# Performance work log

Hardware: AMD Instinct MI355X
Metric: run time of the kernel (lower is better)

The kernel has to match this reference:

```python
import jax, jax.numpy as jnp
import numpy as np

N, E = 50000, 800000          # nodes, edges
F_IN, H, C = 32, 64, 7        # input feats, hidden, classes
EPS = 1e-5                    # BatchNorm eps


def setup_inputs() -> dict:
    key = jax.random.key(0)
    ks = jax.random.split(key, 16)
    inp = {
        "x": jax.random.normal(ks[0], (N, F_IN), jnp.float32),
        "edge_index": jax.random.randint(ks[1], (2, E), 0, N),
        "edge_attr": jax.random.uniform(ks[2], (E, 1), jnp.float32),
    }

    def conv_params(k, cin, cout, i):
        k1, k2 = jax.random.split(k)
        s = 1.0 / np.sqrt(cin)
        inp[f"W{i}"] = jax.random.uniform(k1, (2, cin, cout), jnp.float32, -s, s)  # spline kernel weights
        inp[f"R{i}"] = jax.random.uniform(k2, (cin, cout), jnp.float32, -s, s)     # root weight
        inp[f"B{i}"] = jnp.zeros((cout,), jnp.float32)

    conv_params(ks[3], F_IN, H, 0)
    conv_params(ks[4], H, H, 1)
    conv_params(ks[5], H, C, 2)
    for i in range(2):  # BatchNorm (eval mode: running stats)
        inp[f"G{i}"] = jnp.ones((H,), jnp.float32)
        inp[f"BE{i}"] = jnp.zeros((H,), jnp.float32)
        inp[f"RM{i}"] = 0.1 * jax.random.normal(ks[6 + 2 * i], (H,), jnp.float32)
        inp[f"RV{i}"] = jax.random.uniform(ks[7 + 2 * i], (H,), jnp.float32, 0.5, 1.5)
    return inp


def spline_conv(x, src, dst, u, W, R, B):
    # dim=1, kernel_size=2, degree=1 open B-spline:
    # basis = (1-u, u) with weight indices (0, 1) for u in [0,1).
    basis = jnp.stack([1.0 - u, u], axis=1)               # [E, 2]
    msg = jnp.einsum('ec,ek,kco->eo', x[src], basis, W)    # gather + basis-weighted linear
    agg = jax.ops.segment_sum(msg, dst, num_segments=N)    # scatter-add
    deg = jax.ops.segment_sum(jnp.ones((src.shape[0],), x.dtype), dst, num_segments=N)
    agg = agg / jnp.maximum(deg, 1.0)[:, None]             # aggr='mean' (default)
    return agg + x @ R + B                                 # root weight + bias


def batch_norm(x, g, b, rm, rv):
    return (x - rm) * jax.lax.rsqrt(rv + EPS) * g + b


def reference(x, edge_index, edge_attr,
              W0, R0, B0, W1, R1, B1, W2, R2, B2,
              G0, BE0, RM0, RV0, G1, BE1, RM1, RV1):
    src, dst = edge_index[0], edge_index[1]
    u = edge_attr[:, 0]
    h = spline_conv(x, src, dst, u, W0, R0, B0)
    h = jax.nn.elu(batch_norm(h, G0, BE0, RM0, RV0))
    h = spline_conv(h, src, dst, u, W1, R1, B1)
    h = jax.nn.elu(batch_norm(h, G1, BE1, RM1, RV1))
    h = spline_conv(h, src, dst, u, W2, R2, B2)
    return jax.nn.log_softmax(h, axis=1)
```

## Files before the change

kernel.cpp:

```cpp
#include <hip/hip_runtime.h>
#include <hip/hip_fp16.h>
#include <math.h>

#define NN 50000
#define NE 800000
#define EPSV 1e-5f
#define BSHIFT 7
#define BSIZE 128
#define NB 391
#define CAP 2560

typedef _Float16 h2f   __attribute__((ext_vector_type(2)));
typedef _Float16 f16x8 __attribute__((ext_vector_type(8)));
typedef float    f32x4 __attribute__((ext_vector_type(4)));

__global__ __launch_bounds__(64) void prep_all_kernel(
        const float* __restrict__ W0, const float* __restrict__ R0,
        const float* __restrict__ W1, const float* __restrict__ R1,
        const float* __restrict__ W2, const float* __restrict__ R2,
        const float* __restrict__ B0, const float* __restrict__ B1,
        const float* __restrict__ G0, const float* __restrict__ BE0,
        const float* __restrict__ RM0, const float* __restrict__ RV0,
        const float* __restrict__ G1, const float* __restrict__ BE1,
        const float* __restrict__ RM1, const float* __restrict__ RV1,
        __half* __restrict__ Bf0, __half* __restrict__ Bf1, __half* __restrict__ Bf7,
        float* __restrict__ bn0, float* __restrict__ bn1,
        int* __restrict__ bcursor) {
    int lane = threadIdx.x;
    int bid = blockIdx.x;
    int c = lane & 15;
    int kbase = ((lane >> 4) << 3);
    _Float16 vals[8];
    if (bid < 12) {
        int ks = bid >> 2, nt = bid & 3;
        int n = nt * 16 + c;
#pragma unroll
        for (int j = 0; j < 8; ++j) {
            int kg = ks * 32 + kbase + j;
            float v = (kg < 64) ? W0[(kg & 1) * 2048 + (kg >> 1) * 64 + n]
                                : R0[(kg - 64) * 64 + n];
            vals[j] = (_Float16)v;
        }
        *reinterpret_cast<f16x8*>(Bf0 + ((size_t)(bid * 64 + lane)) * 8) =
            *reinterpret_cast<f16x8*>(vals);
    } else if (bid < 36) {
        int t = bid - 12;
        int ks = t >> 2, nt = t & 3;
        int n = nt * 16 + c;
#pragma unroll
        for (int j = 0; j < 8; ++j) {
            int kg = ks * 32 + kbase + j;
            float v = (kg < 128) ? W1[(kg & 1) * 4096 + (kg >> 1) * 64 + n]
                                 : R1[(kg - 128) * 64 + n];
            vals[j] = (_Float16)v;
        }
        *reinterpret_cast<f16x8*>(Bf1 + ((size_t)(t * 64 + lane)) * 8) =
            *reinterpret_cast<f16x8*>(vals);
    } else if (bid < 40) {
        int ksnt = bid - 36;
        int ks = ksnt >> 1, nt = ksnt & 1;
#pragma unroll
        for (int j = 0; j < 8; ++j) {
            int k = ks * 32 + kbase + j;
            float v = 0.f;
            if (nt == 0) {
                if (c < 7)                 v = W2[k * 7 + c];
                else if (c >= 8 && c < 15) v = W2[448 + k * 7 + (c - 8)];
            } else {
                if (c < 7)                 v = R2[k * 7 + c];
            }
            vals[j] = (_Float16)v;
        }
        *reinterpret_cast<f16x8*>(Bf7 + ((size_t)(ksnt * 64 + lane)) * 8) =
            *reinterpret_cast<f16x8*>(vals);
    } else if (bid == 40) {
        float s = G0[lane] * rsqrtf(RV0[lane] + EPSV);
        bn0[lane] = s;
        bn0[64 + lane] = B0[lane] * s + BE0[lane] - RM0[lane] * s;
    } else if (bid == 41) {
        float s = G1[lane] * rsqrtf(RV1[lane] + EPSV);
        bn1[lane] = s;
        bn1[64 + lane] = B1[lane] * s + BE1[lane] - RM1[lane] * s;
    } else {
        int b = (bid - 42) * 64 + lane;
        if (b < NB) bcursor[b] = b * CAP;
    }
}

__global__ __launch_bounds__(256) void binB_xh_kernel(
        const int* __restrict__ src, const int* __restrict__ dst,
        const float* __restrict__ attr, int* __restrict__ bcursor,
        unsigned* __restrict__ es1su, unsigned char* __restrict__ es1dl, int E,
        const float* __restrict__ x, __half* __restrict__ xh) {
    __shared__ int hist[NB];
    __shared__ int base[NB];
    if (blockIdx.x >= NB) {
        int t = (blockIdx.x - NB) * 256 + threadIdx.x;
        size_t idx = (size_t)t * 8;
        if (idx < (size_t)NN * 32) {
            float4 f0 = *reinterpret_cast<const float4*>(x + idx);
            float4 f1 = *reinterpret_cast<const float4*>(x + idx + 4);
            _Float16 v[8] = {(_Float16)f0.x, (_Float16)f0.y, (_Float16)f0.z, (_Float16)f0.w,
                             (_Float16)f1.x, (_Float16)f1.y, (_Float16)f1.z, (_Float16)f1.w};
            *reinterpret_cast<f16x8*>(xh + idx) = *reinterpret_cast<f16x8*>(v);
        }
        return;
    }
    for (int i = threadIdx.x; i < NB; i += blockDim.x) hist[i] = 0;
    __syncthreads();
    const int chunk = (E + NB - 1) / NB;
    int e0 = blockIdx.x * chunk;
    int e1 = e0 + chunk; if (e1 > E) e1 = E;
    unsigned su[8]; unsigned char dlv[8]; short bv[8];
#pragma unroll
    for (int j = 0; j < 8; ++j) {
        int e = e0 + threadIdx.x + j * 256;
        if (e < e1) {
            int d = dst[e];
            int b = d >> BSHIFT;
            __half uh = __float2half_rn(attr[e]);
            su[j]  = ((unsigned)src[e] << 16) | (unsigned)__half_as_ushort(uh);
            dlv[j] = (unsigned char)(d & (BSIZE - 1));
            bv[j]  = (short)b;
            atomicAdd(&hist[b], 1);
        }
    }
    __syncthreads();
    for (int i = threadIdx.x; i < NB; i += blockDim.x) {
        int cnt = hist[i];
        base[i] = cnt ? atomicAdd(&bcursor[i], cnt) : 0;
        hist[i] = 0;
    }
    __syncthreads();
#pragma unroll
    for (int j = 0; j < 8; ++j) {
        int e = e0 + threadIdx.x + j * 256;
        if (e < e1) {
            int b = bv[j];
            int slot = base[b] + atomicAdd(&hist[b], 1);
            es1su[slot] = su[j];
            es1dl[slot] = dlv[j];
        }
    }
}

__global__ __launch_bounds__(256) void placeC_kernel(const int* __restrict__ bcursor,
                                                     const unsigned* __restrict__ es1su,
                                                     const unsigned char* __restrict__ es1dl,
                                                     int2* __restrict__ rowrange,
                                                     uint2* __restrict__ es8) {
    __shared__ int hist[BSIZE];
    __shared__ int stmp[BSIZE];
    __shared__ int cur[BSIZE];
    int b = blockIdx.x;
    int t = threadIdx.x;
    int bs = b * CAP;
    int be = bcursor[b];
    if (t < BSIZE) hist[t] = 0;
    __syncthreads();
    unsigned su[10]; unsigned char dlv[10];
#pragma unroll
    for (int j = 0; j < 10; ++j) {
        int i = bs + t + j * 256;
        if (i < be) {
            su[j]  = es1su[i];
            dlv[j] = es1dl[i];
            atomicAdd(&hist[dlv[j]], 1);
        }
    }
    __syncthreads();
    if (t < BSIZE) {
        int v = hist[t];
        int incl = v;
#pragma unroll
        for (int o = 1; o < 64; o <<= 1) {
            int nv = __shfl_up(incl, o, 64);
            if ((t & 63) >= o) incl += nv;
        }
        stmp[t] = incl;
    }
    __syncthreads();
    if (t < BSIZE) {
        int excl = stmp[t] - hist[t] + ((t >= 64) ? stmp[63] : 0);
        cur[t] = excl;
        int node = b * BSIZE + t;
        if (node < NN) {
            int2 rr; rr.x = bs + excl; rr.y = bs + excl + hist[t];
            rowrange[node] = rr;
        }
    }
    __syncthreads();
#pragma unroll
    for (int j = 0; j < 10; ++j) {
        int i = bs + t + j * 256;
        if (i < be) {
            unsigned r = su[j];
            int dl = dlv[j];
            int slot = bs + atomicAdd(&cur[dl], 1);
            __half uh = __ushort_as_half((unsigned short)(r & 0xffffu));
            __half2 p = __halves2half2(__hsub(__ushort_as_half((unsigned short)0x3C00u), uh), uh);
            uint2 rec;
            rec.x = r >> 16;
            rec.y = *reinterpret_cast<unsigned*>(&p);
            es8[slot] = rec;
        }
    }
}

__global__ __launch_bounds__(256) void gatherS32_kernel(const int2* __restrict__ rowrange,
                                                        const uint2* __restrict__ es8,
                                                        const __half* __restrict__ xh,
                                                        __half* __restrict__ S, int n_nodes) {
    int n = (blockIdx.x * blockDim.x + threadIdx.x) >> 6;
    int lane = threadIdx.x & 63;
    if (n >= n_nodes) return;
    int2 rr = rowrange[n];
    int beg = __builtin_amdgcn_readfirstlane(rr.x);
    int end = __builtin_amdgcn_readfirstlane(rr.y);
    int c = lane & 31;
    const __half* xb = xh + c;
    float a0 = 0.f, a1 = 0.f, a2 = 0.f, a3 = 0.f;
    float b0 = 0.f, b1 = 0.f, b2 = 0.f, b3 = 0.f;
    int i = beg + (lane >> 5);
    for (; i + 6 < end; i += 8) {
        uint2 q0 = es8[i];
        uint2 q1 = es8[i + 2];
        uint2 q2 = es8[i + 4];
        uint2 q3 = es8[i + 6];
        float x0 = __half2float(xb[(size_t)q0.x << 5]);
        float x1 = __half2float(xb[(size_t)q1.x << 5]);
        float x2 = __half2float(xb[(size_t)q2.x << 5]);
        float x3 = __half2float(xb[(size_t)q3.x << 5]);
        __half2 u0 = __builtin_bit_cast(__half2, q0.y);
        __half2 u1 = __builtin_bit_cast(__half2, q1.y);
        __half2 u2 = __builtin_bit_cast(__half2, q2.y);
        __half2 u3 = __builtin_bit_cast(__half2, q3.y);
        a0 = fmaf(__low2float(u0), x0, a0); b0 = fmaf(__high2float(u0), x0, b0);
        a1 = fmaf(__low2float(u1), x1, a1); b1 = fmaf(__high2float(u1), x1, b1);
        a2 = fmaf(__low2float(u2), x2, a2); b2 = fmaf(__high2float(u2), x2, b2);
        a3 = fmaf(__low2float(u3), x3, a3); b3 = fmaf(__high2float(u3), x3, b3);
    }
    for (; i < end; i += 2) {
        uint2 q = es8[i];
        float xv = __half2float(xb[(size_t)q.x << 5]);
        __half2 u = __builtin_bit_cast(__half2, q.y);
        a0 = fmaf(__low2float(u), xv, a0); b0 = fmaf(__high2float(u), xv, b0);
    }
    float a = (a0 + a1) + (a2 + a3);
    float b = (b0 + b1) + (b2 + b3);
    a += __shfl_xor(a, 32);
    b += __shfl_xor(b, 32);
    float degv = (float)(end - beg);
    if (degv < 1.f) degv = 1.f;
    float inv = 1.f / degv;
    if (lane < 32) {
        reinterpret_cast<__half2*>(S + (size_t)n * 64)[c] = __floats2half2_rn(a * inv, b * inv);
    }
}

__global__ __launch_bounds__(256) void gatherS64_kernel(const int2* __restrict__ rowrange,
                                                        const uint2* __restrict__ es8,
                                                        const __half* __restrict__ ht,
                                                        __half* __restrict__ S, int n_nodes) {
    int n = (blockIdx.x * blockDim.x + threadIdx.x) >> 6;
    int lane = threadIdx.x & 63;
    if (n >= n_nodes) return;
    int2 rr = rowrange[n];
    int beg = __builtin_amdgcn_readfirstlane(rr.x);
    int end = __builtin_amdgcn_readfirstlane(rr.y);
    const __half* xb = ht + lane;
    float a0 = 0.f, a1 = 0.f, a2 = 0.f, a3 = 0.f;
    float b0 = 0.f, b1 = 0.f, b2 = 0.f, b3 = 0.f;
    int i = beg;
    if (i < end && (i & 1)) {
        uint2 q = es8[i];
        float xv = __half2float(xb[(size_t)q.x << 6]);
        __half2 u = __builtin_bit_cast(__half2, q.y);
        a0 = fmaf(__low2float(u), xv, a0); b0 = fmaf(__high2float(u), xv, b0);
        ++i;
    }
    for (; i + 7 < end; i += 8) {
        uint4 p0 = *reinterpret_cast<const uint4*>(es8 + i);
        uint4 p1 = *reinterpret_cast<const uint4*>(es8 + i + 2);
        uint4 p2 = *reinterpret_cast<const uint4*>(es8 + i + 4);
        uint4 p3 = *reinterpret_cast<const uint4*>(es8 + i + 6);
        float x0 = __half2float(xb[(size_t)p0.x << 6]);
        float x1 = __half2float(xb[(size_t)p0.z << 6]);
        float x2 = __half2float(xb[(size_t)p1.x << 6]);
        float x3 = __half2float(xb[(size_t)p1.z << 6]);
        float x4 = __half2float(xb[(size_t)p2.x << 6]);
        float x5 = __half2float(xb[(size_t)p2.z << 6]);
        float x6 = __half2float(xb[(size_t)p3.x << 6]);
        float x7 = __half2float(xb[(size_t)p3.z << 6]);
        __half2 u0 = __builtin_bit_cast(__half2, p0.y);
        __half2 u1 = __builtin_bit_cast(__half2, p0.w);
        __half2 u2 = __builtin_bit_cast(__half2, p1.y);
        __half2 u3 = __builtin_bit_cast(__half2, p1.w);
        __half2 u4 = __builtin_bit_cast(__half2, p2.y);
        __half2 u5 = __builtin_bit_cast(__half2, p2.w);
        __half2 u6 = __builtin_bit_cast(__half2, p3.y);
        __half2 u7 = __builtin_bit_cast(__half2, p3.w);
        a0 = fmaf(__low2float(u0), x0, a0); b0 = fmaf(__high2float(u0), x0, b0);
        a1 = fmaf(__low2float(u1), x1, a1); b1 = fmaf(__high2float(u1), x1, b1);
        a2 = fmaf(__low2float(u2), x2, a2); b2 = fmaf(__high2float(u2), x2, b2);
        a3 = fmaf(__low2float(u3), x3, a3); b3 = fmaf(__high2float(u3), x3, b3);
        a0 = fmaf(__low2float(u4), x4, a0); b0 = fmaf(__high2float(u4), x4, b0);
        a1 = fmaf(__low2float(u5), x5, a1); b1 = fmaf(__high2float(u5), x5, b1);
        a2 = fmaf(__low2float(u6), x6, a2); b2 = fmaf(__high2float(u6), x6, b2);
        a3 = fmaf(__low2float(u7), x7, a3); b3 = fmaf(__high2float(u7), x7, b3);
    }
    for (; i + 1 < end; i += 2) {
        uint4 p = *reinterpret_cast<const uint4*>(es8 + i);
        float x0 = __half2float(xb[(size_t)p.x << 6]);
        float x1 = __half2float(xb[(size_t)p.z << 6]);
        __half2 u0 = __builtin_bit_cast(__half2, p.y);
        __half2 u1 = __builtin_bit_cast(__half2, p.w);
        a0 = fmaf(__low2float(u0), x0, a0); b0 = fmaf(__high2float(u0), x0, b0);
        a1 = fmaf(__low2float(u1), x1, a1); b1 = fmaf(__high2float(u1), x1, b1);
    }
    if (i < end) {
        uint2 q = es8[i];
        float xv = __half2float(xb[(size_t)q.x << 6]);
        __half2 u = __builtin_bit_cast(__half2, q.y);
        a0 = fmaf(__low2float(u), xv, a0); b0 = fmaf(__high2float(u), xv, b0);
    }
    float a = (a0 + a1) + (a2 + a3);
    float b = (b0 + b1) + (b2 + b3);
    float degv = (float)(end - beg);
    if (degv < 1.f) degv = 1.f;
    float inv = 1.f / degv;
    reinterpret_cast<__half2*>(S + (size_t)n * 128)[lane] = __floats2half2_rn(a * inv, b * inv);
}

__global__ __launch_bounds__(256) void gemmL0_kernel(const __half* __restrict__ S,
                                                     const __half* __restrict__ xh,
                                                     const __half* __restrict__ Bf0,
                                                     const float* __restrict__ bn,
                                                     __half* __restrict__ hout, int n_nodes) {
    const int lane = threadIdx.x & 63;
    const int wid  = threadIdx.x >> 6;
    int m0 = (blockIdx.x * 4 + wid) * 16;
    if (m0 >= n_nodes) return;
    f32x4 acc[4];
#pragma unroll
    for (int i = 0; i < 4; ++i) acc[i] = (f32x4){0.f, 0.f, 0.f, 0.f};
    const int arow = m0 + (lane & 15);
    const int koff = ((lane >> 4) << 3);
    const f16x8* bf = reinterpret_cast<const f16x8*>(Bf0);
    const _Float16* sp = (const _Float16*)S  + (size_t)arow * 64 + koff;
    const _Float16* xp = (const _Float16*)xh + (size_t)arow * 32 + koff;
    f16x8 a0 = *reinterpret_cast<const f16x8*>(sp);
    f16x8 a1 = *reinterpret_cast<const f16x8*>(sp + 32);
    f16x8 a2 = *reinterpret_cast<const f16x8*>(xp);
#pragma unroll
    for (int nt = 0; nt < 4; ++nt)
        acc[nt] = __builtin_amdgcn_mfma_f32_16x16x32_f16(a0, bf[nt * 64 + lane], acc[nt], 0, 0, 0);
#pragma unroll
    for (int nt = 0; nt < 4; ++nt)
        acc[nt] = __builtin_amdgcn_mfma_f32_16x16x32_f16(a1, bf[(4 + nt) * 64 + lane], acc[nt], 0, 0, 0);
#pragma unroll
    for (int nt = 0; nt < 4; ++nt)
        acc[nt] = __builtin_amdgcn_mfma_f32_16x16x32_f16(a2, bf[(8 + nt) * 64 + lane], acc[nt], 0, 0, 0);
    const int c_lo  = lane & 15;
    const int rbase = ((lane >> 4) << 2);
#pragma unroll
    for (int nt = 0; nt < 4; ++nt) {
        int cc = nt * 16 + c_lo;
        float sc = bn[cc], sh = bn[64 + cc];
#pragma unroll
        for (int r = 0; r < 4; ++r) {
            int row = m0 + rbase + r;
            float v = acc[nt][r] * sc + sh;
            v = v > 0.f ? v : expm1f(v);
            hout[(size_t)row * 64 + cc] = __float2half(v);
        }
    }
}

__global__ __launch_bounds__(256) void gemmL1_kernel(const __half* __restrict__ S,
                                                     const __half* __restrict__ hin,
                                                     const __half* __restrict__ Bf1,
                                                     const float* __restrict__ bn,
                                                     __half* __restrict__ hout, int n_nodes) {
    const int lane = threadIdx.x & 63;
    const int wid  = threadIdx.x >> 6;
    int m0 = (blockIdx.x * 4 + wid) * 16;
    if (m0 >= n_nodes) return;
    f32x4 acc[4];
#pragma unroll
    for (int i = 0; i < 4; ++i) acc[i] = (f32x4){0.f, 0.f, 0.f, 0.f};
    const int arow = m0 + (lane & 15);
    const int koff = ((lane >> 4) << 3);
    const f16x8* bf = reinterpret_cast<const f16x8*>(Bf1);
    const _Float16* sp = (const _Float16*)S   + (size_t)arow * 128 + koff;
    const _Float16* hp = (const _Float16*)hin + (size_t)arow * 64  + koff;
#pragma unroll
    for (int ks = 0; ks < 6; ++ks) {
        f16x8 av = (ks < 4) ? *reinterpret_cast<const f16x8*>(sp + ks * 32)
                            : *reinterpret_cast<const f16x8*>(hp + (ks - 4) * 32);
#pragma unroll
        for (int nt = 0; nt < 4; ++nt)
            acc[nt] = __builtin_amdgcn_mfma_f32_16x16x32_f16(av, bf[(ks * 4 + nt) * 64 + lane], acc[nt], 0, 0, 0);
    }
    const int c_lo  = lane & 15;
    const int rbase = ((lane >> 4) << 2);
#pragma unroll
    for (int nt = 0; nt < 4; ++nt) {
        int cc = nt * 16 + c_lo;
        float sc = bn[cc], sh = bn[64 + cc];
#pragma unroll
        for (int r = 0; r < 4; ++r) {
            int row = m0 + rbase + r;
            float v = acc[nt][r] * sc + sh;
            v = v > 0.f ? v : expm1f(v);
            hout[(size_t)row * 64 + cc] = __float2half(v);
        }
    }
}

__global__ __launch_bounds__(256) void gemm7_kernel(const __half* __restrict__ h,
                               const __half* __restrict__ Bf7,
                               const float* __restrict__ Bb,
                               __half* __restrict__ Yab7H,
                               float* __restrict__ Z7,
                               int n_nodes) {
    const int lane = threadIdx.x & 63;
    const int wid  = threadIdx.x >> 6;
    int m0 = (blockIdx.x * 4 + wid) * 16;
    if (m0 >= n_nodes) return;

    f32x4 acc[2];
    acc[0] = (f32x4){0.f, 0.f, 0.f, 0.f};
    acc[1] = (f32x4){0.f, 0.f, 0.f, 0.f};
    const int arow = m0 + (lane & 15);
    const int koff = ((lane >> 4) << 3);
    const f16x8* bf = reinterpret_cast<const f16x8*>(Bf7);
#pragma unroll
    for (int ks = 0; ks < 2; ++ks) {
        f16x8 av = *reinterpret_cast<const f16x8*>(
            (const _Float16*)h + (size_t)arow * 64 + ks * 32 + koff);
#pragma unroll
        for (int nt = 0; nt < 2; ++nt) {
            f16x8 bv = bf[(ks * 2 + nt) * 64 + lane];
            acc[nt] = __builtin_amdgcn_mfma_f32_16x16x32_f16(av, bv, acc[nt], 0, 0, 0);
        }
    }
    const int c_lo  = lane & 15;
    const int rbase = ((lane >> 4) << 2);
#pragma unroll
    for (int r = 0; r < 4; ++r) {
        int row = m0 + rbase + r;
        if (c_lo < 7) {
            Yab7H[(size_t)row * 14 + 2 * c_lo] = __float2half(acc[0][r]);
            Z7[(size_t)row * 7 + c_lo] = acc[1][r] + Bb[c_lo];
        } else if (c_lo >= 8 && c_lo < 15) {
            Yab7H[(size_t)row * 14 + 2 * (c_lo - 8) + 1] = __float2half(acc[0][r]);
        }
    }
}

__global__ void gather7_final_kernel(const int2* __restrict__ rowrange,
                                     const uint2* __restrict__ es8,
                                     const __half2* __restrict__ Yab7H,
                                     const float* __restrict__ Z7,
                                     float* __restrict__ out, int n_nodes) {
    int t = blockIdx.x * blockDim.x + threadIdx.x;
    int n = t >> 3;
    int c = t & 7;
    if (n >= n_nodes) return;
    int2 rr = rowrange[n];
    int beg = rr.x, end = rr.y;
    float acc0 = 0.f, acc1 = 0.f, acc2 = 0.f, acc3 = 0.f;
    if (c < 7) {
        int i = beg;
        for (; i + 3 < end; i += 4) {
            uint2 q0 = es8[i];
            uint2 q1 = es8[i + 1];
            uint2 q2 = es8[i + 2];
            uint2 q3 = es8[i + 3];
            __half2 v0 = Yab7H[(size_t)q0.x * 7 + c];
            __half2 v1 = Yab7H[(size_t)q1.x * 7 + c];
            __half2 v2 = Yab7H[(size_t)q2.x * 7 + c];
            __half2 v3 = Yab7H[(size_t)q3.x * 7 + c];
            acc0 = __builtin_amdgcn_fdot2(__builtin_bit_cast(h2f, v0), __builtin_bit_cast(h2f, q0.y), acc0, false);
            acc1 = __builtin_amdgcn_fdot2(__builtin_bit_cast(h2f, v1), __builtin_bit_cast(h2f, q1.y), acc1, false);
            acc2 = __builtin_amdgcn_fdot2(__builtin_bit_cast(h2f, v2), __builtin_bit_cast(h2f, q2.y), acc2, false);
            acc3 = __builtin_amdgcn_fdot2(__builtin_bit_cast(h2f, v3), __builtin_bit_cast(h2f, q3.y), acc3, false);
        }
        for (; i < end; ++i) {
            uint2 q = es8[i];
            __half2 v = Yab7H[(size_t)q.x * 7 + c];
            acc0 = __builtin_amdgcn_fdot2(__builtin_bit_cast(h2f, v), __builtin_bit_cast(h2f, q.y), acc0, false);
        }
    }
    float acc = (acc0 + acc1) + (acc2 + acc3);
    float degv = (float)(end - beg);
    if (degv < 1.f) degv = 1.f;
    float v = (c < 7) ? (acc / degv + Z7[n * 7 + c]) : -1e30f;
    float m = v;
#pragma unroll
    for (int o = 1; o < 8; o <<= 1) m = fmaxf(m, __shfl_xor(m, o, 8));
    float ex = (c < 7) ? expf(v - m) : 0.f;
    float ssum = ex;
#pragma unroll
    for (int o = 1; o < 8; o <<= 1) ssum += __shfl_xor(ssum, o, 8);
    if (c < 7) out[n * 7 + c] = v - m - logf(ssum);
}

extern "C" void kernel_launch(void* const* d_in, const int* in_sizes, int n_in,
                              void* d_out, int out_size, void* d_ws, size_t ws_size,
                              hipStream_t stream) {
    const float* x    = (const float*)d_in[0];
    const int*   ei   = (const int*)d_in[1];
    const float* attr = (const float*)d_in[2];
    const float* W0 = (const float*)d_in[3];
    const float* R0 = (const float*)d_in[4];
    const float* B0 = (const float*)d_in[5];
    const float* W1 = (const float*)d_in[6];
    const float* R1 = (const float*)d_in[7];
    const float* B1 = (const float*)d_in[8];
    const float* W2 = (const float*)d_in[9];
    const float* R2 = (const float*)d_in[10];
    const float* B2 = (const float*)d_in[11];
    const float* G0  = (const float*)d_in[12];
    const float* BE0 = (const float*)d_in[13];
    const float* RM0 = (const float*)d_in[14];
    const float* RV0 = (const float*)d_in[15];
    const float* G1  = (const float*)d_in[16];
    const float* BE1 = (const float*)d_in[17];
    const float* RM1 = (const float*)d_in[18];
    const float* RV1 = (const float*)d_in[19];

    const int* src = ei;
    const int* dst = ei + NE;
    float* out = (float*)d_out;

    char* ws = (char*)d_ws;
    size_t off = 0;
    auto alloc = [&](size_t bytes) { char* p = ws + off; off += (bytes + 255) & ~size_t(255); return p; };
    int*           bcursor  = (int*)          alloc(NB * sizeof(int));
    int2*          rowrange = (int2*)         alloc((size_t)NN * sizeof(int2));
    unsigned*      es1su    = (unsigned*)     alloc((size_t)NB * CAP * sizeof(unsigned));
    unsigned char* es1dl    = (unsigned char*)alloc((size_t)NB * CAP * sizeof(unsigned char));
    uint2*         es8      = (uint2*)        alloc((size_t)NB * CAP * sizeof(uint2));
    __half*        Bf0      = (__half*)       alloc((size_t)12 * 64 * 8 * sizeof(__half));
    __half*        Bf1      = (__half*)       alloc((size_t)24 * 64 * 8 * sizeof(__half));
    __half*        Bf7      = (__half*)       alloc((size_t)4 * 64 * 8 * sizeof(__half));
    float*         bn0      = (float*)        alloc(128 * sizeof(float));
    float*         bn1      = (float*)        alloc(128 * sizeof(float));
    __half*        xh       = (__half*)       alloc((size_t)NN * 32 * sizeof(__half));
    __half*        S        = (__half*)       alloc((size_t)NN * 128 * sizeof(__half));
    __half*        h0       = (__half*)       alloc((size_t)NN * 64 * sizeof(__half));
    __half*        h1       = (__half*)       alloc((size_t)NN * 64 * sizeof(__half));
    __half*        Yab7H    = (__half*)       alloc((size_t)NN * 14 * sizeof(__half));
    float*         Z7       = (float*)        alloc((size_t)NN * 7 * sizeof(float));

    const int B = 256;
    const int gM    = ((NN + 15) / 16 + 3) / 4;
    const int gGath = (NN * 64) / (B);
    const int gN8   = (NN * 8 + B - 1) / B;
    const int gConv = ((NN * 32 / 8) + B - 1) / B;
    const int gPrep = 42 + (NB + 63) / 64;

    prep_all_kernel<<<gPrep, 64, 0, stream>>>(W0, R0, W1, R1, W2, R2, B0, B1,
                                              G0, BE0, RM0, RV0, G1, BE1, RM1, RV1,
                                              Bf0, Bf1, Bf7, bn0, bn1, bcursor);

    binB_xh_kernel<<<NB + gConv, B, 0, stream>>>(src, dst, attr, bcursor, es1su, es1dl, NE, x, xh);

    placeC_kernel<<<NB, B, 0, stream>>>(bcursor, es1su, es1dl, rowrange, es8);

    gatherS32_kernel<<<gGath, B, 0, stream>>>(rowrange, es8, xh, S, NN);
    gemmL0_kernel<<<gM, B, 0, stream>>>(S, xh, Bf0, bn0, h0, NN);

    gatherS64_kernel<<<gGath, B, 0, stream>>>(rowrange, es8, h0, S, NN);
    gemmL1_kernel<<<gM, B, 0, stream>>>(S, h0, Bf1, bn1, h1, NN);

    gemm7_kernel<<<gM, B, 0, stream>>>(h1, Bf7, B2, Yab7H, Z7, NN);
    gather7_final_kernel<<<gN8, B, 0, stream>>>(rowrange, es8, (const __half2*)Yab7H, Z7, out, NN);
}
```

Measured before the change: 209.3 us.

## Fuse layer-1 GEMM with class GEMM via LDS, pad layouts, deepen gather unroll

Merges the layer-1 GEMM and the 7-class projection into one kernel. The ELU output is staged in swizzled LDS instead of being written to and re-read from a global h1 buffer, which also removes one launch. Yab7H and Z7 are padded to power-of-two row strides so gathers use shift/or addressing. The 32-wide gather is unrolled to 16 edges with 8 accumulator pairs and both gathers get an occupancy hint. The cost is more LDS and register pressure and added bounds checks.

```diff
diff --git a/kernel.cpp b/kernel.cpp
--- a/kernel.cpp
+++ b/kernel.cpp
@@ -207,74 +207,97 @@
     }
 }
 
-__global__ __launch_bounds__(256) void gatherS32_kernel(const int2* __restrict__ rowrange,
-                                                        const uint2* __restrict__ es8,
-                                                        const __half* __restrict__ xh,
-                                                        __half* __restrict__ S, int n_nodes) {
+__global__ __launch_bounds__(256, 8) void gatherS32_kernel(const int2* __restrict__ rowrange,
+                                                           const uint2* __restrict__ es8,
+                                                           const __half* __restrict__ xh,
+                                                           __half* __restrict__ S, int n_nodes) {
     int n = (blockIdx.x * blockDim.x + threadIdx.x) >> 6;
     int lane = threadIdx.x & 63;
     if (n >= n_nodes) return;
     int2 rr = rowrange[n];
     int beg = __builtin_amdgcn_readfirstlane(rr.x);
     int end = __builtin_amdgcn_readfirstlane(rr.y);
-    int c = lane & 31;
-    const __half* xb = xh + c;
+    const unsigned c2 = (unsigned)((lane & 31) << 1);
+    const char* xb = (const char*)xh;
     float a0 = 0.f, a1 = 0.f, a2 = 0.f, a3 = 0.f;
+    float a4 = 0.f, a5 = 0.f, a6 = 0.f, a7 = 0.f;
     float b0 = 0.f, b1 = 0.f, b2 = 0.f, b3 = 0.f;
+    float b4 = 0.f, b5 = 0.f, b6 = 0.f, b7 = 0.f;
     int i = beg + (lane >> 5);
-    for (; i + 6 < end; i += 8) {
+    for (; i + 14 < end; i += 16) {
         uint2 q0 = es8[i];
         uint2 q1 = es8[i + 2];
         uint2 q2 = es8[i + 4];
         uint2 q3 = es8[i + 6];
-        float x0 = __half2float(xb[(size_t)q0.x << 5]);
-        float x1 = __half2float(xb[(size_t)q1.x << 5]);
-        float x2 = __half2float(xb[(size_t)q2.x << 5]);
-        float x3 = __half2float(xb[(size_t)q3.x << 5]);
+        uint2 q4 = es8[i + 8];
+        uint2 q5 = es8[i + 10];
+        uint2 q6 = es8[i + 12];
+        uint2 q7 = es8[i + 14];
+        __half x0 = *(const __half*)(xb + ((q0.x << 6) | c2));
+        __half x1 = *(const __half*)(xb + ((q1.x << 6) | c2));
+        __half x2 = *(const __half*)(xb + ((q2.x << 6) | c2));
+        __half x3 = *(const __half*)(xb + ((q3.x << 6) | c2));
+        __half x4 = *(const __half*)(xb + ((q4.x << 6) | c2));
+        __half x5 = *(const __half*)(xb + ((q5.x << 6) | c2));
+        __half x6 = *(const __half*)(xb + ((q6.x << 6) | c2));
+        __half x7 = *(const __half*)(xb + ((q7.x << 6) | c2));
         __half2 u0 = __builtin_bit_cast(__half2, q0.y);
         __half2 u1 = __builtin_bit_cast(__half2, q1.y);
         __half2 u2 = __builtin_bit_cast(__half2, q2.y);
         __half2 u3 = __builtin_bit_cast(__half2, q3.y);
-        a0 = fmaf(__low2float(u0), x0, a0); b0 = fmaf(__high2float(u0), x0, b0);
-        a1 = fmaf(__low2float(u1), x1, a1); b1 = fmaf(__high2float(u1), x1, b1);
-        a2 = fmaf(__low2float(u2), x2, a2); b2 = fmaf(__high2float(u2), x2, b2);
-        a3 = fmaf(__low2float(u3), x3, a3); b3 = fmaf(__high2float(u3), x3, b3);
+        __half2 u4 = __builtin_bit_cast(__half2, q4.y);
+        __half2 u5 = __builtin_bit_cast(__half2, q5.y);
+        __half2 u6 = __builtin_bit_cast(__half2, q6.y);
+        __half2 u7 = __builtin_bit_cast(__half2, q7.y);
+        float f0 = __half2float(x0), f1 = __half2float(x1);
+        float f2 = __half2float(x2), f3 = __half2float(x3);
+        float f4 = __half2float(x4), f5 = __half2float(x5);
+        float f6 = __half2float(x6), f7 = __half2float(x7);
+        a0 = fmaf(__low2float(u0), f0, a0); b0 = fmaf(__high2float(u0), f0, b0);
+        a1 = fmaf(__low2float(u1), f1, a1); b1 = fmaf(__high2float(u1), f1, b1);
+        a2 = fmaf(__low2float(u2), f2, a2); b2 = fmaf(__high2float(u2), f2, b2);
+        a3 = fmaf(__low2float(u3), f3, a3); b3 = fmaf(__high2float(u3), f3, b3);
+        a4 = fmaf(__low2float(u4), f4, a4); b4 = fmaf(__high2float(u4), f4, b4);
+        a5 = fmaf(__low2float(u5), f5, a5); b5 = fmaf(__high2float(u5), f5, b5);
+        a6 = fmaf(__low2float(u6), f6, a6); b6 = fmaf(__high2float(u6), f6, b6);
+        a7 = fmaf(__low2float(u7), f7, a7); b7 = fmaf(__high2float(u7), f7, b7);
     }
     for (; i < end; i += 2) {
         uint2 q = es8[i];
-        float xv = __half2float(xb[(size_t)q.x << 5]);
+        float xv = __half2float(*(const __half*)(xb + ((q.x << 6) | c2)));
         __half2 u = __builtin_bit_cast(__half2, q.y);
         a0 = fmaf(__low2float(u), xv, a0); b0 = fmaf(__high2float(u), xv, b0);
     }
-    float a = (a0 + a1) + (a2 + a3);
-    float b = (b0 + b1) + (b2 + b3);
+    float a = ((a0 + a1) + (a2 + a3)) + ((a4 + a5) + (a6 + a7));
+    float b = ((b0 + b1) + (b2 + b3)) + ((b4 + b5) + (b6 + b7));
     a += __shfl_xor(a, 32);
     b += __shfl_xor(b, 32);
     float degv = (float)(end - beg);
     if (degv < 1.f) degv = 1.f;
     float inv = 1.f / degv;
     if (lane < 32) {
-        reinterpret_cast<__half2*>(S + (size_t)n * 64)[c] = __floats2half2_rn(a * inv, b * inv);
-    }
-}
-
-__global__ __launch_bounds__(256) void gatherS64_kernel(const int2* __restrict__ rowrange,
-                                                        const uint2* __restrict__ es8,
-                                                        const __half* __restrict__ ht,
-                                                        __half* __restrict__ S, int n_nodes) {
+        reinterpret_cast<__half2*>(S + (size_t)n * 64)[lane] = __floats2half2_rn(a * inv, b * inv);
+    }
+}
+
+__global__ __launch_bounds__(256, 8) void gatherS64_kernel(const int2* __restrict__ rowrange,
+                                                           const uint2* __restrict__ es8,
+                                                           const __half* __restrict__ ht,
+                                                           __half* __restrict__ S, int n_nodes) {
     int n = (blockIdx.x * blockDim.x + threadIdx.x) >> 6;
     int lane = threadIdx.x & 63;
     if (n >= n_nodes) return;
     int2 rr = rowrange[n];
     int beg = __builtin_amdgcn_readfirstlane(rr.x);
     int end = __builtin_amdgcn_readfirstlane(rr.y);
-    const __half* xb = ht + lane;
+    const unsigned c2 = (unsigned)(lane << 1);
+    const char* xb = (const char*)ht;
     float a0 = 0.f, a1 = 0.f, a2 = 0.f, a3 = 0.f;
     float b0 = 0.f, b1 = 0.f, b2 = 0.f, b3 = 0.f;
     int i = beg;
     if (i < end && (i & 1)) {
         uint2 q = es8[i];
-        float xv = __half2float(xb[(size_t)q.x << 6]);
+        float xv = __half2float(*(const __half*)(xb + ((q.x << 7) | c2)));
         __half2 u = __builtin_bit_cast(__half2, q.y);
         a0 = fmaf(__low2float(u), xv, a0); b0 = fmaf(__high2float(u), xv, b0);
         ++i;
@@ -284,14 +307,14 @@
         uint4 p1 = *reinterpret_cast<const uint4*>(es8 + i + 2);
         uint4 p2 = *reinterpret_cast<const uint4*>(es8 + i + 4);
         uint4 p3 = *reinterpret_cast<const uint4*>(es8 + i + 6);
-        float x0 = __half2float(xb[(size_t)p0.x << 6]);
-        float x1 = __half2float(xb[(size_t)p0.z << 6]);
-        float x2 = __half2float(xb[(size_t)p1.x << 6]);
-        float x3 = __half2float(xb[(size_t)p1.z << 6]);
-        float x4 = __half2float(xb[(size_t)p2.x << 6]);
-        float x5 = __half2float(xb[(size_t)p2.z << 6]);
-        float x6 = __half2float(xb[(size_t)p3.x << 6]);
-        float x7 = __half2float(xb[(size_t)p3.z << 6]);
+        __half x0 = *(const __half*)(xb + ((p0.x << 7) | c2));
+        __half x1 = *(const __half*)(xb + ((p0.z << 7) | c2));
+        __half x2 = *(const __half*)(xb + ((p1.x << 7) | c2));
+        __half x3 = *(const __half*)(xb + ((p1.z << 7) | c2));
+        __half x4 = *(const __half*)(xb + ((p2.x << 7) | c2));
+        __half x5 = *(const __half*)(xb + ((p2.z << 7) | c2));
+        __half x6 = *(const __half*)(xb + ((p3.x << 7) | c2));
+        __half x7 = *(const __half*)(xb + ((p3.z << 7) | c2));
         __half2 u0 = __builtin_bit_cast(__half2, p0.y);
         __half2 u1 = __builtin_bit_cast(__half2, p0.w);
         __half2 u2 = __builtin_bit_cast(__half2, p1.y);
@@ -300,27 +323,31 @@
         __half2 u5 = __builtin_bit_cast(__half2, p2.w);
         __half2 u6 = __builtin_bit_cast(__half2, p3.y);
         __half2 u7 = __builtin_bit_cast(__half2, p3.w);
-        a0 = fmaf(__low2float(u0), x0, a0); b0 = fmaf(__high2float(u0), x0, b0);
-        a1 = fmaf(__low2float(u1), x1, a1); b1 = fmaf(__high2float(u1), x1, b1);
-        a2 = fmaf(__low2float(u2), x2, a2); b2 = fmaf(__high2float(u2), x2, b2);
-        a3 = fmaf(__low2float(u3), x3, a3); b3 = fmaf(__high2float(u3), x3, b3);
-        a0 = fmaf(__low2float(u4), x4, a0); b0 = fmaf(__high2float(u4), x4, b0);
-        a1 = fmaf(__low2float(u5), x5, a1); b1 = fmaf(__high2float(u5), x5, b1);
-        a2 = fmaf(__low2float(u6), x6, a2); b2 = fmaf(__high2float(u6), x6, b2);
-        a3 = fmaf(__low2float(u7), x7, a3); b3 = fmaf(__high2float(u7), x7, b3);
+        float f0 = __half2float(x0), f1 = __half2float(x1);
+        float f2 = __half2float(x2), f3 = __half2float(x3);
+        float f4 = __half2float(x4), f5 = __half2float(x5);
+        float f6 = __half2float(x6), f7 = __half2float(x7);
+        a0 = fmaf(__low2float(u0), f0, a0); b0 = fmaf(__high2float(u0), f0, b0);
+        a1 = fmaf(__low2float(u1), f1, a1); b1 = fmaf(__high2float(u1), f1, b1);
+        a2 = fmaf(__low2float(u2), f2, a2); b2 = fmaf(__high2float(u2), f2, b2);
+        a3 = fmaf(__low2float(u3), f3, a3); b3 = fmaf(__high2float(u3), f3, b3);
+        a0 = fmaf(__low2float(u4), f4, a0); b0 = fmaf(__high2float(u4), f4, b0);
+        a1 = fmaf(__low2float(u5), f5, a1); b1 = fmaf(__high2float(u5), f5, b1);
+        a2 = fmaf(__low2float(u6), f6, a2); b2 = fmaf(__high2float(u6), f6, b2);
+        a3 = fmaf(__low2float(u7), f7, a3); b3 = fmaf(__high2float(u7), f7, b3);
     }
     for (; i + 1 < end; i += 2) {
         uint4 p = *reinterpret_cast<const uint4*>(es8 + i);
-        float x0 = __half2float(xb[(size_t)p.x << 6]);
-        float x1 = __half2float(xb[(size_t)p.z << 6]);
+        float f0 = __half2float(*(const __half*)(xb + ((p.x << 7) | c2)));
+        float f1 = __half2float(*(const __half*)(xb + ((p.z << 7) | c2)));
         __half2 u0 = __builtin_bit_cast(__half2, p.y);
         __half2 u1 = __builtin_bit_cast(__half2, p.w);
-        a0 = fmaf(__low2float(u0), x0, a0); b0 = fmaf(__high2float(u0), x0, b0);
-        a1 = fmaf(__low2float(u1), x1, a1); b1 = fmaf(__high2float(u1), x1, b1);
+        a0 = fmaf(__low2float(u0), f0, a0); b0 = fmaf(__high2float(u0), f0, b0);
+        a1 = fmaf(__low2float(u1), f1, a1); b1 = fmaf(__high2float(u1), f1, b1);
     }
     if (i < end) {
         uint2 q = es8[i];
-        float xv = __half2float(xb[(size_t)q.x << 6]);
+        float xv = __half2float(*(const __half*)(xb + ((q.x << 7) | c2)));
         __half2 u = __builtin_bit_cast(__half2, q.y);
         a0 = fmaf(__low2float(u), xv, a0); b0 = fmaf(__high2float(u), xv, b0);
     }
@@ -370,18 +397,25 @@
 #pragma unroll
         for (int r = 0; r < 4; ++r) {
             int row = m0 + rbase + r;
-            float v = acc[nt][r] * sc + sh;
-            v = v > 0.f ? v : expm1f(v);
-            hout[(size_t)row * 64 + cc] = __float2half(v);
-        }
-    }
-}
-
-__global__ __launch_bounds__(256) void gemmL1_kernel(const __half* __restrict__ S,
-                                                     const __half* __restrict__ hin,
-                                                     const __half* __restrict__ Bf1,
-                                                     const float* __restrict__ bn,
-                                                     __half* __restrict__ hout, int n_nodes) {
+            if (row < n_nodes) {
+                float v = acc[nt][r] * sc + sh;
+                v = v > 0.f ? v : expm1f(v);
+                hout[(size_t)row * 64 + cc] = __float2half(v);
+            }
+        }
+    }
+}
+
+__global__ __launch_bounds__(256) void gemmL1_7_kernel(const __half* __restrict__ S,
+                                                       const __half* __restrict__ hin,
+                                                       const __half* __restrict__ Bf1,
+                                                       const __half* __restrict__ Bf7,
+                                                       const float* __restrict__ bn,
+                                                       const float* __restrict__ Bb2,
+                                                       __half* __restrict__ Yab7H,
+                                                       float* __restrict__ Z7,
+                                                       int n_nodes) {
+    __shared__ __align__(16) char ldsH[64 * 128];
     const int lane = threadIdx.x & 63;
     const int wid  = threadIdx.x >> 6;
     int m0 = (blockIdx.x * 4 + wid) * 16;
@@ -390,7 +424,8 @@
 #pragma unroll
     for (int i = 0; i < 4; ++i) acc[i] = (f32x4){0.f, 0.f, 0.f, 0.f};
     const int arow = m0 + (lane & 15);
-    const int koff = ((lane >> 4) << 3);
+    const int g = lane >> 4;
+    const int koff = g << 3;
     const f16x8* bf = reinterpret_cast<const f16x8*>(Bf1);
     const _Float16* sp = (const _Float16*)S   + (size_t)arow * 128 + koff;
     const _Float16* hp = (const _Float16*)hin + (size_t)arow * 64  + koff;
@@ -410,51 +445,36 @@
         float sc = bn[cc], sh = bn[64 + cc];
 #pragma unroll
         for (int r = 0; r < 4; ++r) {
-            int row = m0 + rbase + r;
             float v = acc[nt][r] * sc + sh;
             v = v > 0.f ? v : expm1f(v);
-            hout[(size_t)row * 64 + cc] = __float2half(v);
-        }
-    }
-}
-
-__global__ __launch_bounds__(256) void gemm7_kernel(const __half* __restrict__ h,
-                               const __half* __restrict__ Bf7,
-                               const float* __restrict__ Bb,
-                               __half* __restrict__ Yab7H,
-                               float* __restrict__ Z7,
-                               int n_nodes) {
-    const int lane = threadIdx.x & 63;
-    const int wid  = threadIdx.x >> 6;
-    int m0 = (blockIdx.x * 4 + wid) * 16;
-    if (m0 >= n_nodes) return;
-
-    f32x4 acc[2];
-    acc[0] = (f32x4){0.f, 0.f, 0.f, 0.f};
-    acc[1] = (f32x4){0.f, 0.f, 0.f, 0.f};
-    const int arow = m0 + (lane & 15);
-    const int koff = ((lane >> 4) << 3);
-    const f16x8* bf = reinterpret_cast<const f16x8*>(Bf7);
+            int rl = wid * 16 + rbase + r;
+            *reinterpret_cast<__half*>(ldsH + ((rl * 128 + cc * 2) ^ ((rl & 7) << 4))) = __float2half(v);
+        }
+    }
+
+    const int rowl = wid * 16 + (lane & 15);
+    const int swz = (rowl & 7) << 4;
+    f32x4 acc7[2];
+    acc7[0] = (f32x4){0.f, 0.f, 0.f, 0.f};
+    acc7[1] = (f32x4){0.f, 0.f, 0.f, 0.f};
+    const f16x8* bf7 = reinterpret_cast<const f16x8*>(Bf7);
 #pragma unroll
     for (int ks = 0; ks < 2; ++ks) {
-        f16x8 av = *reinterpret_cast<const f16x8*>(
-            (const _Float16*)h + (size_t)arow * 64 + ks * 32 + koff);
-#pragma unroll
-        for (int nt = 0; nt < 2; ++nt) {
-            f16x8 bv = bf[(ks * 2 + nt) * 64 + lane];
-            acc[nt] = __builtin_amdgcn_mfma_f32_16x16x32_f16(av, bv, acc[nt], 0, 0, 0);
-        }
-    }
-    const int c_lo  = lane & 15;
-    const int rbase = ((lane >> 4) << 2);
+        f16x8 av = *reinterpret_cast<const f16x8*>(ldsH + ((rowl * 128 + ks * 64 + g * 16) ^ swz));
+#pragma unroll
+        for (int nt = 0; nt < 2; ++nt)
+            acc7[nt] = __builtin_amdgcn_mfma_f32_16x16x32_f16(av, bf7[(ks * 2 + nt) * 64 + lane], acc7[nt], 0, 0, 0);
+    }
 #pragma unroll
     for (int r = 0; r < 4; ++r) {
         int row = m0 + rbase + r;
-        if (c_lo < 7) {
-            Yab7H[(size_t)row * 14 + 2 * c_lo] = __float2half(acc[0][r]);
-            Z7[(size_t)row * 7 + c_lo] = acc[1][r] + Bb[c_lo];
-        } else if (c_lo >= 8 && c_lo < 15) {
-            Yab7H[(size_t)row * 14 + 2 * (c_lo - 8) + 1] = __float2half(acc[0][r]);
+        if (row < n_nodes) {
+            if (c_lo < 7) {
+                Yab7H[((size_t)row << 4) + 2 * c_lo] = __float2half(acc7[0][r]);
+                Z7[((size_t)row << 3) + c_lo] = acc7[1][r] + Bb2[c_lo];
+            } else if (c_lo >= 8 && c_lo < 15) {
+                Yab7H[((size_t)row << 4) + 2 * (c_lo - 8) + 1] = __float2half(acc7[0][r]);
+            }
         }
     }
 }
@@ -470,33 +490,47 @@
     if (n >= n_nodes) return;
     int2 rr = rowrange[n];
     int beg = rr.x, end = rr.y;
+    const unsigned c4 = (unsigned)(c << 2);
+    const char* yb = (const char*)Yab7H;
     float acc0 = 0.f, acc1 = 0.f, acc2 = 0.f, acc3 = 0.f;
     if (c < 7) {
         int i = beg;
-        for (; i + 3 < end; i += 4) {
+        for (; i + 7 < end; i += 8) {
             uint2 q0 = es8[i];
             uint2 q1 = es8[i + 1];
             uint2 q2 = es8[i + 2];
             uint2 q3 = es8[i + 3];
-            __half2 v0 = Yab7H[(size_t)q0.x * 7 + c];
-            __half2 v1 = Yab7H[(size_t)q1.x * 7 + c];
-            __half2 v2 = Yab7H[(size_t)q2.x * 7 + c];
-            __half2 v3 = Yab7H[(size_t)q3.x * 7 + c];
+            uint2 q4 = es8[i + 4];
+            uint2 q5 = es8[i + 5];
+            uint2 q6 = es8[i + 6];
+            uint2 q7 = es8[i + 7];
+            __half2 v0 = *(const __half2*)(yb + ((q0.x << 5) | c4));
+            __half2 v1 = *(const __half2*)(yb + ((q1.x << 5) | c4));
+            __half2 v2 = *(const __half2*)(yb + ((q2.x << 5) | c4));
+            __half2 v3 = *(const __half2*)(yb + ((q3.x << 5) | c4));
+            __half2 v4 = *(const __half2*)(yb + ((q4.x << 5) | c4));
+            __half2 v5 = *(const __half2*)(yb + ((q5.x << 5) | c4));
+            __half2 v6 = *(const __half2*)(yb + ((q6.x << 5) | c4));
+            __half2 v7 = *(const __half2*)(yb + ((q7.x << 5) | c4));
             acc0 = __builtin_amdgcn_fdot2(__builtin_bit_cast(h2f, v0), __builtin_bit_cast(h2f, q0.y), acc0, false);
             acc1 = __builtin_amdgcn_fdot2(__builtin_bit_cast(h2f, v1), __builtin_bit_cast(h2f, q1.y), acc1, false);
             acc2 = __builtin_amdgcn_fdot2(__builtin_bit_cast(h2f, v2), __builtin_bit_cast(h2f, q2.y), acc2, false);
             acc3 = __builtin_amdgcn_fdot2(__builtin_bit_cast(h2f, v3), __builtin_bit_cast(h2f, q3.y), acc3, false);
+            acc0 = __builtin_amdgcn_fdot2(__builtin_bit_cast(h2f, v4), __builtin_bit_cast(h2f, q4.y), acc0, false);
+            acc1 = __builtin_amdgcn_fdot2(__builtin_bit_cast(h2f, v5), __builtin_bit_cast(h2f, q5.y), acc1, false);
+            acc2 = __builtin_amdgcn_fdot2(__builtin_bit_cast(h2f, v6), __builtin_bit_cast(h2f, q6.y), acc2, false);
+            acc3 = __builtin_amdgcn_fdot2(__builtin_bit_cast(h2f, v7), __builtin_bit_cast(h2f, q7.y), acc3, false);
         }
         for (; i < end; ++i) {
             uint2 q = es8[i];
-            __half2 v = Yab7H[(size_t)q.x * 7 + c];
+            __half2 v = *(const __half2*)(yb + ((q.x << 5) | c4));
             acc0 = __builtin_amdgcn_fdot2(__builtin_bit_cast(h2f, v), __builtin_bit_cast(h2f, q.y), acc0, false);
         }
     }
     float acc = (acc0 + acc1) + (acc2 + acc3);
     float degv = (float)(end - beg);
     if (degv < 1.f) degv = 1.f;
-    float v = (c < 7) ? (acc / degv + Z7[n * 7 + c]) : -1e30f;
+    float v = (c < 7) ? (acc / degv + Z7[(n << 3) + c]) : -1e30f;
     float m = v;
 #pragma unroll
     for (int o = 1; o < 8; o <<= 1) m = fmaxf(m, __shfl_xor(m, o, 8));
@@ -548,16 +582,15 @@
     __half*        Bf7      = (__half*)       alloc((size_t)4 * 64 * 8 * sizeof(__half));
     float*         bn0      = (float*)        alloc(128 * sizeof(float));
     float*         bn1      = (float*)        alloc(128 * sizeof(float));
-    __half*        xh       = (__half*)       alloc((size_t)NN * 32 * sizeof(__half));
-    __half*        S        = (__half*)       alloc((size_t)NN * 128 * sizeof(__half));
-    __half*        h0       = (__half*)       alloc((size_t)NN * 64 * sizeof(__half));
-    __half*        h1       = (__half*)       alloc((size_t)NN * 64 * sizeof(__half));
-    __half*        Yab7H    = (__half*)       alloc((size_t)NN * 14 * sizeof(__half));
-    float*         Z7       = (float*)        alloc((size_t)NN * 7 * sizeof(float));
+    __half*        xh       = (__half*)       alloc((size_t)(NN + 64) * 32 * sizeof(__half));
+    __half*        S        = (__half*)       alloc((size_t)(NN + 64) * 128 * sizeof(__half));
+    __half*        h0       = (__half*)       alloc((size_t)(NN + 64) * 64 * sizeof(__half));
+    __half*        Yab7H    = (__half*)       alloc((size_t)NN * 16 * sizeof(__half));
+    float*         Z7       = (float*)        alloc((size_t)NN * 8 * sizeof(float));
 
     const int B = 256;
     const int gM    = ((NN + 15) / 16 + 3) / 4;
-    const int gGath = (NN * 64) / (B);
+    const int gGath = (NN * 64) / B;
     const int gN8   = (NN * 8 + B - 1) / B;
     const int gConv = ((NN * 32 / 8) + B - 1) / B;
     const int gPrep = 42 + (NB + 63) / 64;
@@ -574,8 +607,7 @@
     gemmL0_kernel<<<gM, B, 0, stream>>>(S, xh, Bf0, bn0, h0, NN);
 
     gatherS64_kernel<<<gGath, B, 0, stream>>>(rowrange, es8, h0, S, NN);
-    gemmL1_kernel<<<gM, B, 0, stream>>>(S, h0, Bf1, bn1, h1, NN);
-
-    gemm7_kernel<<<gM, B, 0, stream>>>(h1, Bf7, B2, Yab7H, Z7, NN);
+    gemmL1_7_kernel<<<gM, B, 0, stream>>>(S, h0, Bf1, Bf7, bn1, B2, Yab7H, Z7, NN);
+
     gather7_final_kernel<<<gN8, B, 0, stream>>>(rowrange, es8, (const __half2*)Yab7H, Z7, out, NN);
 }
```

Result: no change. 209.6 us (+0.1%).
